# Kernel optimization log

Hardware: AMD Instinct MI355X
Metric: run time of the kernel (lower is better)

The kernel has to match this reference:

```python
import jax, jax.numpy as jnp
import numpy as np

NBINS = 256  # skimage threshold_otsu default


def _otsu_threshold(x):
    """Global Otsu threshold over the whole array, matching skimage.filters.threshold_otsu."""
    counts, edges = jnp.histogram(x.reshape(-1), bins=NBINS)
    counts = counts.astype(jnp.float32)
    centers = 0.5 * (edges[:-1] + edges[1:])  # [NBINS]

    # class probabilities / weights for all candidate thresholds
    w1 = jnp.cumsum(counts)                       # weight of class <= t
    w2 = jnp.cumsum(counts[::-1])[::-1]           # weight of class > t
    csum = jnp.cumsum(counts * centers)
    csum_rev = jnp.cumsum((counts * centers)[::-1])[::-1]
    m1 = csum / jnp.maximum(w1, 1.0)              # class means (guard empty bins)
    m2 = csum_rev / jnp.maximum(w2, 1.0)

    # between-class variance at each split point
    var12 = w1[:-1] * w2[1:] * (m1[:-1] - m2[1:]) ** 2  # [NBINS-1]
    idx = jnp.argmax(var12)
    return centers[idx]


def setup_inputs() -> dict:
    key = jax.random.key(0)
    inputs = jax.random.normal(key, (16, 1024, 2048, 1), dtype=jnp.float32)
    return {"inputs": inputs}


def reference(inputs) -> jnp.ndarray:
    x = inputs.astype(jnp.float32)
    thresh = _otsu_threshold(x)
    # ((image > thresh) * 1).astype(float32)
    return (x > thresh).astype(jnp.float32)
```

## Files before the change

### kernel.cpp

```cpp
#include <hip/hip_runtime.h>
#include <stdint.h>

#define NBINS 256
#define NCOPY 32
#define GRID 2048
#define TPB 256
#define HOFF 4
#define MOFF 512
#define XOFF (512 + GRID)

__device__ __forceinline__ float edge_at(int i, float minv, float delta) {
    return __fadd_rn(__fmul_rn((float)i, delta), minv);
}

__device__ __forceinline__ float min4(float4 v) {
    return fminf(fminf(v.x, v.y), fminf(v.z, v.w));
}
__device__ __forceinline__ float max4(float4 v) {
    return fmaxf(fmaxf(v.x, v.y), fmaxf(v.z, v.w));
}


__global__ void __launch_bounds__(TPB) k_minmax(const float* __restrict__ in,
                                                int n, uint32_t* ws) {
    float* fws = (float*)ws;
    int n4 = n >> 2;
    int chunk = (n4 + GRID - 1) / GRID;
    int start = blockIdx.x * chunk;
    int end = start + chunk; if (end > n4) end = n4;
    const float4* in4 = (const float4*)in;
    float vmin = INFINITY, vmax = -INFINITY;

    int i = start + threadIdx.x;
    for (; i + 7 * TPB < end; i += 8 * TPB) {
        float4 v0 = in4[i];
        float4 v1 = in4[i + TPB];
        float4 v2 = in4[i + 2 * TPB];
        float4 v3 = in4[i + 3 * TPB];
        float4 v4 = in4[i + 4 * TPB];
        float4 v5 = in4[i + 5 * TPB];
        float4 v6 = in4[i + 6 * TPB];
        float4 v7 = in4[i + 7 * TPB];
        float mn0 = fminf(fminf(min4(v0), min4(v1)), fminf(min4(v2), min4(v3)));
        float mn1 = fminf(fminf(min4(v4), min4(v5)), fminf(min4(v6), min4(v7)));
        float mx0 = fmaxf(fmaxf(max4(v0), max4(v1)), fmaxf(max4(v2), max4(v3)));
        float mx1 = fmaxf(fmaxf(max4(v4), max4(v5)), fmaxf(max4(v6), max4(v7)));
        vmin = fminf(vmin, fminf(mn0, mn1));
        vmax = fmaxf(vmax, fmaxf(mx0, mx1));
    }
    for (; i < end; i += TPB) {
        float4 v = in4[i];
        vmin = fminf(vmin, min4(v));
        vmax = fmaxf(vmax, max4(v));
    }
    for (int j = (n4 << 2) + blockIdx.x * TPB + threadIdx.x; j < n; j += GRID * TPB) {
        float v = in[j];
        vmin = fminf(vmin, v);
        vmax = fmaxf(vmax, v);
    }
#pragma unroll
    for (int off = 32; off > 0; off >>= 1) {
        vmin = fminf(vmin, __shfl_down(vmin, off));
        vmax = fmaxf(vmax, __shfl_down(vmax, off));
    }
    __shared__ float smin[4], smax[4];
    int wave = threadIdx.x >> 6, lane = threadIdx.x & 63;
    if (lane == 0) { smin[wave] = vmin; smax[wave] = vmax; }
    __syncthreads();
    if (threadIdx.x == 0) {
        float m = fminf(fminf(smin[0], smin[1]), fminf(smin[2], smin[3]));
        float M = fmaxf(fmaxf(smax[0], smax[1]), fmaxf(smax[2], smax[3]));
        fws[MOFF + blockIdx.x] = m;
        fws[XOFF + blockIdx.x] = M;
    }
    if (blockIdx.x == 0) ws[HOFF + threadIdx.x] = 0;
}

__device__ __forceinline__ int bin_of(float v, float minv, float invd) {
    float t = (v - minv) * invd;
    t = fminf(fmaxf(t, 0.0f), 255.0f);
    return (int)t;
}

__device__ __forceinline__ void hist4(float4 q, float minv, float invd,
                                      uint32_t* h, int c) {
    atomicAdd(&h[bin_of(q.x, minv, invd) * NCOPY + c], 1u);
    atomicAdd(&h[bin_of(q.y, minv, invd) * NCOPY + c], 1u);
    atomicAdd(&h[bin_of(q.z, minv, invd) * NCOPY + c], 1u);
    atomicAdd(&h[bin_of(q.w, minv, invd) * NCOPY + c], 1u);
}

__global__ void __launch_bounds__(TPB) k_hist(const float* __restrict__ in,
                                              int n, uint32_t* ws) {
    __shared__ uint32_t h[NBINS * NCOPY];
    float* hf = (float*)h;
    float* fws = (float*)ws;

    float lmin = INFINITY, lmax = -INFINITY;
    for (int k = threadIdx.x; k < GRID; k += TPB) {
        lmin = fminf(lmin, fws[MOFF + k]);
        lmax = fmaxf(lmax, fws[XOFF + k]);
    }
#pragma unroll
    for (int off = 32; off > 0; off >>= 1) {
        lmin = fminf(lmin, __shfl_down(lmin, off));
        lmax = fmaxf(lmax, __shfl_down(lmax, off));
    }
    int wave = threadIdx.x >> 6, lane = threadIdx.x & 63;
    if (lane == 0) { hf[wave] = lmin; hf[8 + wave] = lmax; }
    __syncthreads();
    float minv = fminf(fminf(hf[0], hf[1]), fminf(hf[2], hf[3]));
    float maxv = fmaxf(fmaxf(hf[8], hf[9]), fmaxf(hf[10], hf[11]));
    float invd = __fdiv_rn(256.0f, __fsub_rn(maxv, minv));
    __syncthreads();
    for (int i = threadIdx.x; i < NBINS * NCOPY; i += TPB) h[i] = 0;
    __syncthreads();

    int c = threadIdx.x & (NCOPY - 1);
    int n4 = n >> 2;
    int chunk = (n4 + GRID - 1) / GRID;
    int start = blockIdx.x * chunk;
    int end = start + chunk; if (end > n4) end = n4;
    const float4* in4 = (const float4*)in;
    int i = start + threadIdx.x;
    for (; i + 3 * TPB < end; i += 4 * TPB) {
        float4 q0 = in4[i];
        float4 q1 = in4[i + TPB];
        float4 q2 = in4[i + 2 * TPB];
        float4 q3 = in4[i + 3 * TPB];
        hist4(q0, minv, invd, h, c);
        hist4(q1, minv, invd, h, c);
        hist4(q2, minv, invd, h, c);
        hist4(q3, minv, invd, h, c);
    }
    for (; i < end; i += TPB) {
        hist4(in4[i], minv, invd, h, c);
    }
    for (int j = (n4 << 2) + blockIdx.x * TPB + threadIdx.x; j < n; j += GRID * TPB) {
        atomicAdd(&h[bin_of(in[j], minv, invd) * NCOPY + c], 1u);
    }
    __syncthreads();
    for (int b = threadIdx.x; b < NBINS; b += TPB) {
        uint32_t s = 0;
#pragma unroll
        for (int k = 0; k < NCOPY; ++k) s += h[b * NCOPY + k];
        if (s) atomicAdd(&ws[HOFF + b], s);
    }
}

__global__ void __launch_bounds__(TPB) k_bin(const float* __restrict__ in,
                                             float* __restrict__ out,
                                             int n, const uint32_t* __restrict__ ws) {
    __shared__ float cnt[NBINS], ctr[NBINS], w1[NBINS], w2[NBINS],
                     cs[NBINS], csr[NBINS], scan[NBINS], tsh[1];
    const float* fws = (const float*)ws;
    {
        int i = threadIdx.x;
        float lmin = INFINITY, lmax = -INFINITY;
        for (int k = i; k < GRID; k += TPB) {
            lmin = fminf(lmin, fws[MOFF + k]);
            lmax = fmaxf(lmax, fws[XOFF + k]);
        }
#pragma unroll
        for (int off = 32; off > 0; off >>= 1) {
            lmin = fminf(lmin, __shfl_down(lmin, off));
            lmax = fmaxf(lmax, __shfl_down(lmax, off));
        }
        int wave = i >> 6, lane = i & 63;
        if (lane == 0) { scan[wave] = lmin; scan[8 + wave] = lmax; }
        __syncthreads();
        float minv = fminf(fminf(scan[0], scan[1]), fminf(scan[2], scan[3]));
        float maxv = fmaxf(fmaxf(scan[8], scan[9]), fmaxf(scan[10], scan[11]));
        float delta = __fdiv_rn(__fsub_rn(maxv, minv), 256.0f);
        __syncthreads();

        cnt[i] = (float)ws[HOFF + i];
        float e0 = edge_at(i, minv, delta);
        float e1 = edge_at(i + 1, minv, delta);
        ctr[i] = __fmul_rn(0.5f, __fadd_rn(e0, e1));
        __syncthreads();

        scan[i] = cnt[i]; __syncthreads();
        for (int off = 1; off < NBINS; off <<= 1) {
            float v = scan[i];
            if (i >= off) v = __fadd_rn(scan[i - off], v);
            __syncthreads(); scan[i] = v; __syncthreads();
        }
        w1[i] = scan[i]; __syncthreads();

        scan[i] = __fmul_rn(cnt[i], ctr[i]); __syncthreads();
        for (int off = 1; off < NBINS; off <<= 1) {
            float v = scan[i];
            if (i >= off) v = __fadd_rn(scan[i - off], v);
            __syncthreads(); scan[i] = v; __syncthreads();
        }
        cs[i] = scan[i]; __syncthreads();

        scan[i] = cnt[i]; __syncthreads();
        for (int off = 1; off < NBINS; off <<= 1) {
            float v = scan[i];
            if (i + off < NBINS) v = __fadd_rn(v, scan[i + off]);
            __syncthreads(); scan[i] = v; __syncthreads();
        }
        w2[i] = scan[i]; __syncthreads();

        scan[i] = __fmul_rn(cnt[i], ctr[i]); __syncthreads();
        for (int off = 1; off < NBINS; off <<= 1) {
            float v = scan[i];
            if (i + off < NBINS) v = __fadd_rn(v, scan[i + off]);
            __syncthreads(); scan[i] = v; __syncthreads();
        }
        csr[i] = scan[i]; __syncthreads();

        if (i < NBINS - 1) {
            float m1 = __fdiv_rn(cs[i], fmaxf(w1[i], 1.0f));
            float m2 = __fdiv_rn(csr[i + 1], fmaxf(w2[i + 1], 1.0f));
            float d = __fsub_rn(m1, m2);
            float sq = __fmul_rn(d, d);
            scan[i] = __fmul_rn(__fmul_rn(w1[i], w2[i + 1]), sq);
        }
        __syncthreads();
        if (i == 0) {
            int best = 0; float bv = scan[0];
            for (int k = 1; k < NBINS - 1; ++k) {
                float v = scan[k];
                if (v > bv) { bv = v; best = k; }
            }
            tsh[0] = ctr[best];
        }
        __syncthreads();
    }
    float t = tsh[0];

    int n4 = n >> 2;
    int chunk = (n4 + GRID - 1) / GRID;
    int start = blockIdx.x * chunk;
    int end = start + chunk; if (end > n4) end = n4;
    const float4* in4 = (const float4*)in;
    float4* out4 = (float4*)out;
    int i = start + threadIdx.x;
    for (; i + 3 * TPB < end; i += 4 * TPB) {
        float4 v0 = in4[i];
        float4 v1 = in4[i + TPB];
        float4 v2 = in4[i + 2 * TPB];
        float4 v3 = in4[i + 3 * TPB];
        float4 r0, r1, r2, r3;
        r0.x = v0.x > t ? 1.0f : 0.0f; r0.y = v0.y > t ? 1.0f : 0.0f;
        r0.z = v0.z > t ? 1.0f : 0.0f; r0.w = v0.w > t ? 1.0f : 0.0f;
        r1.x = v1.x > t ? 1.0f : 0.0f; r1.y = v1.y > t ? 1.0f : 0.0f;
        r1.z = v1.z > t ? 1.0f : 0.0f; r1.w = v1.w > t ? 1.0f : 0.0f;
        r2.x = v2.x > t ? 1.0f : 0.0f; r2.y = v2.y > t ? 1.0f : 0.0f;
        r2.z = v2.z > t ? 1.0f : 0.0f; r2.w = v2.w > t ? 1.0f : 0.0f;
        r3.x = v3.x > t ? 1.0f : 0.0f; r3.y = v3.y > t ? 1.0f : 0.0f;
        r3.z = v3.z > t ? 1.0f : 0.0f; r3.w = v3.w > t ? 1.0f : 0.0f;
        out4[i] = r0;
        out4[i + TPB] = r1;
        out4[i + 2 * TPB] = r2;
        out4[i + 3 * TPB] = r3;
    }
    for (; i < end; i += TPB) {
        float4 v = in4[i];
        float4 r;
        r.x = v.x > t ? 1.0f : 0.0f;
        r.y = v.y > t ? 1.0f : 0.0f;
        r.z = v.z > t ? 1.0f : 0.0f;
        r.w = v.w > t ? 1.0f : 0.0f;
        out4[i] = r;
    }
    for (int j = (n4 << 2) + blockIdx.x * TPB + threadIdx.x; j < n; j += GRID * TPB) {
        out[j] = in[j] > t ? 1.0f : 0.0f;
    }
}

extern "C" void kernel_launch(void* const* d_in, const int* in_sizes, int n_in,
                              void* d_out, int out_size, void* d_ws, size_t ws_size,
                              hipStream_t stream) {
    const float* in = (const float*)d_in[0];
    float* out = (float*)d_out;
    uint32_t* ws = (uint32_t*)d_ws;
    int n = in_sizes[0];

    hipLaunchKernelGGL(k_minmax, dim3(GRID), dim3(TPB), 0, stream, in, n, ws);
    hipLaunchKernelGGL(k_hist, dim3(GRID), dim3(TPB), 0, stream, in, n, ws);
    hipLaunchKernelGGL(k_bin, dim3(GRID), dim3(TPB), 0, stream, in, out, n, ws);
}
```

Measured before the change: 149.7 us.

## Pack per-element bin index and center bit in histogram pass for final binarize

The histogram kernel now also writes, for each float4, a packed 32-bit word of four 8-bit bin indices plus a byte of above-bin-center bits into the workspace. The final kernel reads these 5 bytes per four elements instead of 16 bytes of input, and decides the output by comparing the bin index against the chosen Otsu bin. This cuts read traffic in the last pass but adds write traffic in the histogram pass, and the histogram loop loses its 4-way unroll. The packed path runs only when the workspace is large enough, otherwise it falls back to the direct kernel.

```diff
diff --git a/kernel.cpp b/kernel.cpp
--- a/kernel.cpp
+++ b/kernel.cpp
@@ -8,18 +8,17 @@
 #define HOFF 4
 #define MOFF 512
 #define XOFF (512 + GRID)
+#define PKOFF 8192
 
 __device__ __forceinline__ float edge_at(int i, float minv, float delta) {
     return __fadd_rn(__fmul_rn((float)i, delta), minv);
 }
-
 __device__ __forceinline__ float min4(float4 v) {
     return fminf(fminf(v.x, v.y), fminf(v.z, v.w));
 }
 __device__ __forceinline__ float max4(float4 v) {
     return fmaxf(fmaxf(v.x, v.y), fmaxf(v.z, v.w));
 }
-
 
 __global__ void __launch_bounds__(TPB) k_minmax(const float* __restrict__ in,
                                                 int n, uint32_t* ws) {
@@ -68,10 +67,8 @@
     if (lane == 0) { smin[wave] = vmin; smax[wave] = vmax; }
     __syncthreads();
     if (threadIdx.x == 0) {
-        float m = fminf(fminf(smin[0], smin[1]), fminf(smin[2], smin[3]));
-        float M = fmaxf(fmaxf(smax[0], smax[1]), fmaxf(smax[2], smax[3]));
-        fws[MOFF + blockIdx.x] = m;
-        fws[XOFF + blockIdx.x] = M;
+        fws[MOFF + blockIdx.x] = fminf(fminf(smin[0], smin[1]), fminf(smin[2], smin[3]));
+        fws[XOFF + blockIdx.x] = fmaxf(fmaxf(smax[0], smax[1]), fmaxf(smax[2], smax[3]));
     }
     if (blockIdx.x == 0) ws[HOFF + threadIdx.x] = 0;
 }
@@ -82,16 +79,18 @@
     return (int)t;
 }
 
-__device__ __forceinline__ void hist4(float4 q, float minv, float invd,
-                                      uint32_t* h, int c) {
-    atomicAdd(&h[bin_of(q.x, minv, invd) * NCOPY + c], 1u);
-    atomicAdd(&h[bin_of(q.y, minv, invd) * NCOPY + c], 1u);
-    atomicAdd(&h[bin_of(q.z, minv, invd) * NCOPY + c], 1u);
-    atomicAdd(&h[bin_of(q.w, minv, invd) * NCOPY + c], 1u);
+__device__ __forceinline__ uint32_t binbit(float v, float minv, float invd,
+                                           float delta, uint32_t* bit) {
+    int j = bin_of(v, minv, invd);
+    float e0 = edge_at(j, minv, delta);
+    float e1 = edge_at(j + 1, minv, delta);
+    float ctr = __fmul_rn(0.5f, __fadd_rn(e0, e1));
+    *bit = (v > ctr) ? 1u : 0u;
+    return (uint32_t)j;
 }
 
 __global__ void __launch_bounds__(TPB) k_hist(const float* __restrict__ in,
-                                              int n, uint32_t* ws) {
+                                              int n, uint32_t* ws, int packed) {
     __shared__ uint32_t h[NBINS * NCOPY];
     float* hf = (float*)h;
     float* fws = (float*)ws;
@@ -112,6 +111,7 @@
     float minv = fminf(fminf(hf[0], hf[1]), fminf(hf[2], hf[3]));
     float maxv = fmaxf(fmaxf(hf[8], hf[9]), fmaxf(hf[10], hf[11]));
     float invd = __fdiv_rn(256.0f, __fsub_rn(maxv, minv));
+    float delta = __fdiv_rn(__fsub_rn(maxv, minv), 256.0f);
     __syncthreads();
     for (int i = threadIdx.x; i < NBINS * NCOPY; i += TPB) h[i] = 0;
     __syncthreads();
@@ -122,19 +122,24 @@
     int start = blockIdx.x * chunk;
     int end = start + chunk; if (end > n4) end = n4;
     const float4* in4 = (const float4*)in;
-    int i = start + threadIdx.x;
-    for (; i + 3 * TPB < end; i += 4 * TPB) {
-        float4 q0 = in4[i];
-        float4 q1 = in4[i + TPB];
-        float4 q2 = in4[i + 2 * TPB];
-        float4 q3 = in4[i + 3 * TPB];
-        hist4(q0, minv, invd, h, c);
-        hist4(q1, minv, invd, h, c);
-        hist4(q2, minv, invd, h, c);
-        hist4(q3, minv, invd, h, c);
-    }
-    for (; i < end; i += TPB) {
-        hist4(in4[i], minv, invd, h, c);
+    uint32_t* bins = ws + PKOFF;
+    uint8_t* bits8 = (uint8_t*)(ws + PKOFF + n4);
+
+    for (int i = start + threadIdx.x; i < end; i += TPB) {
+        float4 q = in4[i];
+        uint32_t b0, b1, b2, b3;
+        uint32_t j0 = binbit(q.x, minv, invd, delta, &b0);
+        uint32_t j1 = binbit(q.y, minv, invd, delta, &b1);
+        uint32_t j2 = binbit(q.z, minv, invd, delta, &b2);
+        uint32_t j3 = binbit(q.w, minv, invd, delta, &b3);
+        atomicAdd(&h[j0 * NCOPY + c], 1u);
+        atomicAdd(&h[j1 * NCOPY + c], 1u);
+        atomicAdd(&h[j2 * NCOPY + c], 1u);
+        atomicAdd(&h[j3 * NCOPY + c], 1u);
+        if (packed) {
+            bins[i] = j0 | (j1 << 8) | (j2 << 16) | (j3 << 24);
+            bits8[i] = (uint8_t)(b0 | (b1 << 1) | (b2 << 2) | (b3 << 3));
+        }
     }
     for (int j = (n4 << 2) + blockIdx.x * TPB + threadIdx.x; j < n; j += GRID * TPB) {
         atomicAdd(&h[bin_of(in[j], minv, invd) * NCOPY + c], 1u);
@@ -148,89 +153,131 @@
     }
 }
 
-__global__ void __launch_bounds__(TPB) k_bin(const float* __restrict__ in,
-                                             float* __restrict__ out,
-                                             int n, const uint32_t* __restrict__ ws) {
+__device__ __forceinline__ void otsu_prologue(const uint32_t* __restrict__ ws,
+                                              int* best_out, float* thresh_out) {
     __shared__ float cnt[NBINS], ctr[NBINS], w1[NBINS], w2[NBINS],
-                     cs[NBINS], csr[NBINS], scan[NBINS], tsh[1];
+                     cs[NBINS], csr[NBINS], scan[NBINS];
+    __shared__ int sbest;
     const float* fws = (const float*)ws;
-    {
-        int i = threadIdx.x;
-        float lmin = INFINITY, lmax = -INFINITY;
-        for (int k = i; k < GRID; k += TPB) {
-            lmin = fminf(lmin, fws[MOFF + k]);
-            lmax = fmaxf(lmax, fws[XOFF + k]);
+    int i = threadIdx.x;
+
+    float lmin = INFINITY, lmax = -INFINITY;
+    for (int k = i; k < GRID; k += TPB) {
+        lmin = fminf(lmin, fws[MOFF + k]);
+        lmax = fmaxf(lmax, fws[XOFF + k]);
+    }
+#pragma unroll
+    for (int off = 32; off > 0; off >>= 1) {
+        lmin = fminf(lmin, __shfl_down(lmin, off));
+        lmax = fmaxf(lmax, __shfl_down(lmax, off));
+    }
+    int wave = i >> 6, lane = i & 63;
+    if (lane == 0) { scan[wave] = lmin; scan[8 + wave] = lmax; }
+    __syncthreads();
+    float minv = fminf(fminf(scan[0], scan[1]), fminf(scan[2], scan[3]));
+    float maxv = fmaxf(fmaxf(scan[8], scan[9]), fmaxf(scan[10], scan[11]));
+    float delta = __fdiv_rn(__fsub_rn(maxv, minv), 256.0f);
+    __syncthreads();
+
+    cnt[i] = (float)ws[HOFF + i];
+    float e0 = edge_at(i, minv, delta);
+    float e1 = edge_at(i + 1, minv, delta);
+    ctr[i] = __fmul_rn(0.5f, __fadd_rn(e0, e1));
+    __syncthreads();
+
+    scan[i] = cnt[i]; __syncthreads();
+    for (int off = 1; off < NBINS; off <<= 1) {
+        float v = scan[i];
+        if (i >= off) v = __fadd_rn(scan[i - off], v);
+        __syncthreads(); scan[i] = v; __syncthreads();
+    }
+    w1[i] = scan[i]; __syncthreads();
+
+    scan[i] = __fmul_rn(cnt[i], ctr[i]); __syncthreads();
+    for (int off = 1; off < NBINS; off <<= 1) {
+        float v = scan[i];
+        if (i >= off) v = __fadd_rn(scan[i - off], v);
+        __syncthreads(); scan[i] = v; __syncthreads();
+    }
+    cs[i] = scan[i]; __syncthreads();
+
+    scan[i] = cnt[i]; __syncthreads();
+    for (int off = 1; off < NBINS; off <<= 1) {
+        float v = scan[i];
+        if (i + off < NBINS) v = __fadd_rn(v, scan[i + off]);
+        __syncthreads(); scan[i] = v; __syncthreads();
+    }
+    w2[i] = scan[i]; __syncthreads();
+
+    scan[i] = __fmul_rn(cnt[i], ctr[i]); __syncthreads();
+    for (int off = 1; off < NBINS; off <<= 1) {
+        float v = scan[i];
+        if (i + off < NBINS) v = __fadd_rn(v, scan[i + off]);
+        __syncthreads(); scan[i] = v; __syncthreads();
+    }
+    csr[i] = scan[i]; __syncthreads();
+
+    if (i < NBINS - 1) {
+        float m1 = __fdiv_rn(cs[i], fmaxf(w1[i], 1.0f));
+        float m2 = __fdiv_rn(csr[i + 1], fmaxf(w2[i + 1], 1.0f));
+        float d = __fsub_rn(m1, m2);
+        scan[i] = __fmul_rn(__fmul_rn(w1[i], w2[i + 1]), __fmul_rn(d, d));
+    }
+    __syncthreads();
+    if (i == 0) {
+        int best = 0; float bv = scan[0];
+        for (int k = 1; k < NBINS - 1; ++k) {
+            float v = scan[k];
+            if (v > bv) { bv = v; best = k; }
         }
-#pragma unroll
-        for (int off = 32; off > 0; off >>= 1) {
-            lmin = fminf(lmin, __shfl_down(lmin, off));
-            lmax = fmaxf(lmax, __shfl_down(lmax, off));
-        }
-        int wave = i >> 6, lane = i & 63;
-        if (lane == 0) { scan[wave] = lmin; scan[8 + wave] = lmax; }
-        __syncthreads();
-        float minv = fminf(fminf(scan[0], scan[1]), fminf(scan[2], scan[3]));
-        float maxv = fmaxf(fmaxf(scan[8], scan[9]), fmaxf(scan[10], scan[11]));
-        float delta = __fdiv_rn(__fsub_rn(maxv, minv), 256.0f);
-        __syncthreads();
-
-        cnt[i] = (float)ws[HOFF + i];
-        float e0 = edge_at(i, minv, delta);
-        float e1 = edge_at(i + 1, minv, delta);
-        ctr[i] = __fmul_rn(0.5f, __fadd_rn(e0, e1));
-        __syncthreads();
-
-        scan[i] = cnt[i]; __syncthreads();
-        for (int off = 1; off < NBINS; off <<= 1) {
-            float v = scan[i];
-            if (i >= off) v = __fadd_rn(scan[i - off], v);
-            __syncthreads(); scan[i] = v; __syncthreads();
-        }
-        w1[i] = scan[i]; __syncthreads();
-
-        scan[i] = __fmul_rn(cnt[i], ctr[i]); __syncthreads();
-        for (int off = 1; off < NBINS; off <<= 1) {
-            float v = scan[i];
-            if (i >= off) v = __fadd_rn(scan[i - off], v);
-            __syncthreads(); scan[i] = v; __syncthreads();
-        }
-        cs[i] = scan[i]; __syncthreads();
-
-        scan[i] = cnt[i]; __syncthreads();
-        for (int off = 1; off < NBINS; off <<= 1) {
-            float v = scan[i];
-            if (i + off < NBINS) v = __fadd_rn(v, scan[i + off]);
-            __syncthreads(); scan[i] = v; __syncthreads();
-        }
-        w2[i] = scan[i]; __syncthreads();
-
-        scan[i] = __fmul_rn(cnt[i], ctr[i]); __syncthreads();
-        for (int off = 1; off < NBINS; off <<= 1) {
-            float v = scan[i];
-            if (i + off < NBINS) v = __fadd_rn(v, scan[i + off]);
-            __syncthreads(); scan[i] = v; __syncthreads();
-        }
-        csr[i] = scan[i]; __syncthreads();
-
-        if (i < NBINS - 1) {
-            float m1 = __fdiv_rn(cs[i], fmaxf(w1[i], 1.0f));
-            float m2 = __fdiv_rn(csr[i + 1], fmaxf(w2[i + 1], 1.0f));
-            float d = __fsub_rn(m1, m2);
-            float sq = __fmul_rn(d, d);
-            scan[i] = __fmul_rn(__fmul_rn(w1[i], w2[i + 1]), sq);
-        }
-        __syncthreads();
-        if (i == 0) {
-            int best = 0; float bv = scan[0];
-            for (int k = 1; k < NBINS - 1; ++k) {
-                float v = scan[k];
-                if (v > bv) { bv = v; best = k; }
-            }
-            tsh[0] = ctr[best];
-        }
-        __syncthreads();
-    }
-    float t = tsh[0];
+        sbest = best;
+        scan[0] = ctr[best];
+    }
+    __syncthreads();
+    *best_out = sbest;
+    *thresh_out = scan[0];
+    __syncthreads();
+}
+
+__global__ void __launch_bounds__(TPB) k_bin_packed(const float* __restrict__ in,
+                                                    float* __restrict__ out,
+                                                    int n,
+                                                    const uint32_t* __restrict__ ws) {
+    int best; float t;
+    otsu_prologue(ws, &best, &t);
+
+    int n4 = n >> 2;
+    int chunk = (n4 + GRID - 1) / GRID;
+    int start = blockIdx.x * chunk;
+    int end = start + chunk; if (end > n4) end = n4;
+    const uint32_t* bins = ws + PKOFF;
+    const uint8_t* bits8 = (const uint8_t*)(ws + PKOFF + n4);
+    float4* out4 = (float4*)out;
+    uint32_t ubest = (uint32_t)best;
+
+    for (int i = start + threadIdx.x; i < end; i += TPB) {
+        uint32_t u = bins[i];
+        uint32_t bt = bits8[i];
+        float4 r;
+        uint32_t j0 = u & 255u, j1 = (u >> 8) & 255u,
+                 j2 = (u >> 16) & 255u, j3 = (u >> 24) & 255u;
+        r.x = (j0 > ubest || (j0 == ubest && (bt & 1u))) ? 1.0f : 0.0f;
+        r.y = (j1 > ubest || (j1 == ubest && (bt & 2u))) ? 1.0f : 0.0f;
+        r.z = (j2 > ubest || (j2 == ubest && (bt & 4u))) ? 1.0f : 0.0f;
+        r.w = (j3 > ubest || (j3 == ubest && (bt & 8u))) ? 1.0f : 0.0f;
+        out4[i] = r;
+    }
+    for (int j = (n4 << 2) + blockIdx.x * TPB + threadIdx.x; j < n; j += GRID * TPB) {
+        out[j] = in[j] > t ? 1.0f : 0.0f;
+    }
+}
+
+__global__ void __launch_bounds__(TPB) k_bin_direct(const float* __restrict__ in,
+                                                    float* __restrict__ out,
+                                                    int n,
+                                                    const uint32_t* __restrict__ ws) {
+    int best; float t;
+    otsu_prologue(ws, &best, &t);
 
     int n4 = n >> 2;
     int chunk = (n4 + GRID - 1) / GRID;
@@ -279,8 +326,18 @@
     float* out = (float*)d_out;
     uint32_t* ws = (uint32_t*)d_ws;
     int n = in_sizes[0];
+    int n4 = n >> 2;
+
+    size_t need = (size_t)(PKOFF + (size_t)n4) * 4 + (size_t)n4;
+    int packed = (ws_size >= need) ? 1 : 0;
 
     hipLaunchKernelGGL(k_minmax, dim3(GRID), dim3(TPB), 0, stream, in, n, ws);
-    hipLaunchKernelGGL(k_hist, dim3(GRID), dim3(TPB), 0, stream, in, n, ws);
-    hipLaunchKernelGGL(k_bin, dim3(GRID), dim3(TPB), 0, stream, in, out, n, ws);
-}
+    hipLaunchKernelGGL(k_hist, dim3(GRID), dim3(TPB), 0, stream, in, n, ws, packed);
+    if (packed) {
+        hipLaunchKernelGGL(k_bin_packed, dim3(GRID), dim3(TPB), 0, stream,
+                           in, out, n, ws);
+    } else {
+        hipLaunchKernelGGL(k_bin_direct, dim3(GRID), dim3(TPB), 0, stream,
+                           in, out, n, ws);
+    }
+}
```

Measured after the change: 144.0 us. 1.04x faster.
